# Kernel tuning notes

Hardware: AMD Instinct MI355X
Metric: run time of the kernel (lower is better)

Reference implementation:

```python
import jax, jax.numpy as jnp
import numpy as np
from jax import lax

B = 2
K = 3          # class_num (out_channels)
EPS = 1e-5


def group_norm(x, gamma, beta, groups):
    # x: [B, C, D, W, H]
    b, c, d, w, h = x.shape
    xg = x.reshape(b, groups, c // groups, d, w, h)
    mu = xg.mean(axis=(2, 3, 4, 5), keepdims=True)
    var = xg.var(axis=(2, 3, 4, 5), keepdims=True)
    xg = (xg - mu) * lax.rsqrt(var + EPS)
    x = xg.reshape(b, c, d, w, h)
    return x * gamma[None, :, None, None, None] + beta[None, :, None, None, None]


def setup_inputs() -> dict:
    key = jax.random.key(0)
    ks = jax.random.split(key, 16)
    s = 0.02
    inp = {
        "x_e": jax.random.normal(ks[0], (B, 128, 24, 24, 24), jnp.float32),
        "pred": jax.random.normal(ks[1], (B, 32, 96, 96, 96), jnp.float32),
        # GAP head params
        "gn_g": jnp.ones((128,), jnp.float32),
        "gn_b": jnp.zeros((128,), jnp.float32),
        "gap_w": jax.random.normal(ks[2], (256, 128, 3, 3, 3), jnp.float32) * s,
        "gap_b": jnp.zeros((256,), jnp.float32),
        # controller_first: Conv3d(512,512,1) == Linear
        "w_cf": jax.random.normal(ks[3], (512, 512), jnp.float32) * s,
        "b_cf": jnp.zeros((512,), jnp.float32),
        # controller: Conv3d(512,256,1)
        "w_c": jax.random.normal(ks[4], (256, 512), jnp.float32) * s,
        "b_c": jnp.zeros((256,), jnp.float32),
        # ProAttention(256, reduction=16): Linear(256,16) -> ReLU -> Linear(16,32)
        "w_a1": jax.random.normal(ks[5], (16, 256), jnp.float32) * s,
        "b_a1": jnp.zeros((16,), jnp.float32),
        "w_a2": jax.random.normal(ks[6], (32, 16), jnp.float32) * s,
        "b_a2": jnp.zeros((32,), jnp.float32),
        # organ embedding [K, 256]
        "emb": jax.random.normal(ks[7], (K, 256), jnp.float32),
        # three seg heads Conv3d(32,1,1): stacked [K, 32] weight, [K] bias
        "w_seg": jax.random.normal(ks[8], (K, 32), jnp.float32) * s,
        "b_seg": jnp.zeros((K,), jnp.float32),
    }
    return inp


def reference(x_e, pred, gn_g, gn_b, gap_w, gap_b, w_cf, b_cf, w_c, b_c,
              w_a1, b_a1, w_a2, b_a2, emb, w_seg, b_seg):
    # GAP(x_e.detach()): GroupNorm -> ReLU -> Conv3d(128->256, k3, s2, VALID) -> global avg pool
    xe = lax.stop_gradient(x_e)
    g = jax.nn.relu(group_norm(xe, gn_g, gn_b, groups=16))
    g = lax.conv_general_dilated(g, gap_w, window_strides=(2, 2, 2), padding="VALID",
                                 dimension_numbers=("NCDHW", "OIDHW", "NCDHW"))
    g = g + gap_b[None, :, None, None, None]
    x_feat = g.mean(axis=(2, 3, 4))                       # [B, 256]

    # per-sample: cat(repeat(x_feat), task_encoding) -> 1x1 conv heads, vectorized over B and K
    x_cond = jnp.concatenate(
        [jnp.broadcast_to(x_feat[:, None, :], (B, K, 256)),
         jnp.broadcast_to(emb[None, :, :], (B, K, 256))], axis=-1)          # [B, K, 512]
    p = jax.nn.relu(jnp.einsum("bkc,oc->bko", x_cond, w_cf) + b_cf)          # [B, K, 512]
    p_out = p                                                                 # returned as p_out in original
    c = jnp.einsum("bkc,oc->bko", p, w_c) + b_c                              # [B, K, 256]
    hid = jax.nn.relu(jnp.einsum("bkc,oc->bko", c, w_a1) + b_a1)             # [B, K, 16]
    gate = jax.nn.sigmoid(jnp.einsum("bkc,oc->bko", hid, w_a2) + b_a2)       # [B, K, 32]

    # out_k = Conv1x1_k(gate_k * pred) = sum_c gate[b,k,c]*w_seg[k,c]*pred[b,c] + b_seg[k]
    eff_w = gate * w_seg[None, :, :]                                          # [B, K, 32]
    logits = jnp.einsum("bkc,bcdwh->bkdwh", eff_w, pred) + b_seg[None, :, None, None, None]
    return logits  # [B, 3, 96, 96, 96]  (p_out available as intermediate `p`)
```

## Files before the change

kernel.cpp:

```cpp
#include <hip/hip_runtime.h>
#include <hip/hip_bf16.h>


#define NSPAT 13824
#define P4    221184

#define WS_STATSPART 0
#define WS_WINS      1024
#define WS_XF        28672
#define WS_P         29184
#define WS_C         32256
#define WS_EFFW      33792
#define WS_BAR       33984
#define WS_SINK      33992

__device__ __forceinline__ void spin_barrier(int* bar, int nb) {
  __syncthreads();
  if (threadIdx.x == 0) {
    __threadfence();
    int gen = atomicAdd(&bar[1], 0);
    int old = atomicAdd(&bar[0], 1);
    if (old == nb - 1) {
      atomicExch(&bar[0], 0);
      __threadfence();
      atomicAdd(&bar[1], 1);
    } else {
      while (atomicAdd(&bar[1], 0) == gen) __builtin_amdgcn_s_sleep(8);
    }
    __threadfence();
  }
  __syncthreads();
}

__global__ __launch_bounds__(256) void k1_stats_kernel(
    const float* __restrict__ x, const float* __restrict__ gap_w,
    const float* __restrict__ w_cf, const float* __restrict__ w_c,
    const float* __restrict__ w_a1, const float* __restrict__ emb,
    float* __restrict__ ws) {
  if (blockIdx.x == 0 && threadIdx.x == 0)
    atomicExch(&((int*)(ws + WS_BAR))[0], 0);
  if (blockIdx.x >= 512) {
    float s = 0.f;
    int tid = (blockIdx.x - 512) * 256 + threadIdx.x;
    const float4* g4 = (const float4*)gap_w;
    for (int i = tid; i < 221184; i += 16384) { float4 v = g4[i]; s += v.x + v.w; }
    const float4* a4 = (const float4*)w_cf;
    for (int i = tid; i < 65536;  i += 16384) { float4 v = a4[i]; s += v.x + v.w; }
    const float4* c4 = (const float4*)w_c;
    for (int i = tid; i < 32768;  i += 16384) { float4 v = c4[i]; s += v.x + v.w; }
    if (tid < 1024) { float4 v = ((const float4*)w_a1)[tid]; s += v.x; }
    if (tid < 192)  { float4 v = ((const float4*)emb)[tid];  s += v.x; }
    if (s == 1.2345e30f) ws[WS_SINK] = s;
    return;
  }
  int blk = blockIdx.x;
  const float4* p = (const float4*)(x + (size_t)blk * 6912);
  float s = 0.f, ss = 0.f;
  for (int i = threadIdx.x; i < 1728; i += 256) {
    float4 v = p[i];
    s  += v.x + v.y + v.z + v.w;
    ss += v.x*v.x + v.y*v.y + v.z*v.z + v.w*v.w;
  }
  #pragma unroll
  for (int off = 32; off; off >>= 1) {
    s  += __shfl_down(s, off);
    ss += __shfl_down(ss, off);
  }
  __shared__ float a[4], b2[4];
  int wid = threadIdx.x >> 6, lane = threadIdx.x & 63;
  if (lane == 0) { a[wid] = s; b2[wid] = ss; }
  __syncthreads();
  if (threadIdx.x == 0) {
    float2 r;
    r.x = a[0] + a[1] + a[2] + a[3];
    r.y = b2[0] + b2[1] + b2[2] + b2[3];
    ((float2*)(ws + WS_STATSPART))[blk] = r;
  }
}

__global__ __launch_bounds__(256) void k2_winsum_kernel(
    const float* __restrict__ x, const float* __restrict__ gn_g,
    const float* __restrict__ gn_b, float* __restrict__ ws) {
  int task = blockIdx.x;
  int zq = task & 3;
  int bc = task >> 2;
  int b = bc >> 7, c = bc & 127;
  int bg = b * 16 + (c >> 3);
  const float2* sp = (const float2*)(ws + WS_STATSPART) + bg * 16;
  float S = 0.f, SS = 0.f;
  #pragma unroll
  for (int j = 0; j < 16; j++) { float2 r = sp[j]; S += r.x; SS += r.y; }
  float mu   = S * (1.f / 110592.f);
  float var  = SS * (1.f / 110592.f) - mu * mu;
  float rstd = rsqrtf(var + 1e-5f);
  float ga = gn_g[c] * rstd;
  float be = gn_b[c] - mu * ga;

  __shared__ float smem[4140];
  int t = threadIdx.x;
  int nz     = (zq < 3) ? 3 : 2;
  int planes = 2 * nz + 1;
  int startf = zq * 3456;
  int nf4    = planes * 144;
  const float4* p = (const float4*)(x + (size_t)bc * NSPAT + startf);
  float4* l4 = (float4*)smem;
  for (int i = t; i < nf4; i += 256) {
    float4 v = p[i];
    float4 r;
    r.x = fmaxf(v.x * ga + be, 0.f);
    r.y = fmaxf(v.y * ga + be, 0.f);
    r.z = fmaxf(v.z * ga + be, 0.f);
    r.w = fmaxf(v.w * ga + be, 0.f);
    l4[i] = r;
  }
  __syncthreads();

  float acc[27];
  #pragma unroll
  for (int k = 0; k < 27; k++) acc[k] = 0.f;
  int npos = nz * 121;
  for (int pidx = t; pidx < npos; pidx += 256) {
    int zl = pidx / 121, rem = pidx % 121;
    int y = rem / 11, xx = rem % 11;
    int base = zl * 1152 + y * 48 + xx * 2;
    #pragma unroll
    for (int kz = 0; kz < 3; kz++)
      #pragma unroll
      for (int ky = 0; ky < 3; ky++)
        #pragma unroll
        for (int kx = 0; kx < 3; kx++)
          acc[kz * 9 + ky * 3 + kx] += smem[base + kz * 576 + ky * 24 + kx];
  }
  #pragma unroll
  for (int k = 0; k < 27; k++)
    for (int off = 32; off; off >>= 1)
      acc[k] += __shfl_down(acc[k], off);
  float* part = smem + 4032;
  __syncthreads();
  int wid = t >> 6, lane = t & 63;
  if (lane == 0)
    #pragma unroll
    for (int k = 0; k < 27; k++) part[wid * 27 + k] = acc[k];
  __syncthreads();
  if (t < 27) {
    float v = part[t] + part[27 + t] + part[54 + t] + part[81 + t];
    ws[WS_WINS + task * 27 + t] = v;
  }
}

__global__ __launch_bounds__(256) void k3_chain_kernel(
    const float* __restrict__ gap_w, const float* __restrict__ gap_b,
    const float* __restrict__ w_cf,  const float* __restrict__ b_cf,
    const float* __restrict__ w_c,   const float* __restrict__ b_c,
    const float* __restrict__ w_a1,  const float* __restrict__ b_a1,
    const float* __restrict__ w_a2,  const float* __restrict__ b_a2,
    const float* __restrict__ emb,   const float* __restrict__ w_seg,
    float* ws) {
  __shared__ float smem[3456];
  int* bar = (int*)(ws + WS_BAR);
  const int t   = threadIdx.x;
  const int blk = blockIdx.x;

  {
    int b = blk >> 6;
    int oc = blk & 63;
    const float* wp = ws + WS_WINS + b * 13824;
    for (int i = t; i < 3456; i += 256) {
      int c = i / 27, k = i - c * 27;
      const float* q = wp + c * 108 + k;
      smem[i] = q[0] + q[27] + q[54] + q[81];
    }
    __syncthreads();
    int olocal = t >> 6;
    int lane = t & 63;
    int o = oc * 4 + olocal;
    const float4* w4 = (const float4*)(gap_w + (size_t)o * 3456);
    const float4* s4 = (const float4*)smem;
    float acc = 0.f;
    for (int i = lane; i < 864; i += 64) {
      float4 wv = w4[i], sv = s4[i];
      acc += wv.x * sv.x + wv.y * sv.y + wv.z * sv.z + wv.w * sv.w;
    }
    #pragma unroll
    for (int off = 32; off; off >>= 1) acc += __shfl_down(acc, off);
    if (lane == 0) ws[WS_XF + b * 256 + o] = acc * (1.f / 1331.f) + gap_b[o];
  }
  spin_barrier(bar, 128);

  {
    for (int i = t; i < 1280; i += 256)
      smem[i] = (i < 512) ? ws[WS_XF + i] : emb[i - 512];
    __syncthreads();
    int r = t >> 6, lane = t & 63;
    int o = blk * 4 + r;
    const float4* w4  = (const float4*)(w_cf + (size_t)o * 512);
    const float4* xf4 = (const float4*)smem;
    const float4* em4 = (const float4*)(smem + 512);
    float4 wlo = w4[lane], whi = w4[lane + 64];
    float acc[6];
    #pragma unroll
    for (int bk = 0; bk < 6; bk++) {
      int b = (bk >= 3), k = bk - b * 3;
      float4 xv = xf4[b * 64 + lane];
      float4 ev = em4[k * 64 + lane];
      acc[bk] = wlo.x*xv.x + wlo.y*xv.y + wlo.z*xv.z + wlo.w*xv.w
              + whi.x*ev.x + whi.y*ev.y + whi.z*ev.z + whi.w*ev.w;
    }
    #pragma unroll
    for (int bk = 0; bk < 6; bk++)
      #pragma unroll
      for (int off = 32; off; off >>= 1)
        acc[bk] += __shfl_down(acc[bk], off);
    if (lane == 0) {
      float bb = b_cf[o];
      #pragma unroll
      for (int bk = 0; bk < 6; bk++)
        ws[WS_P + bk * 512 + o] = fmaxf(acc[bk] + bb, 0.f);
    }
  }
  spin_barrier(bar, 128);

  {
    for (int i = t; i < 3072; i += 256) smem[i] = ws[WS_P + i];
    __syncthreads();
    if (t < 128) {
      int r = t >> 6, lane = t & 63;
      int o = blk * 2 + r;
      const float4* w4 = (const float4*)(w_c + (size_t)o * 512);
      const float4* p4 = (const float4*)smem;
      float4 wlo = w4[lane], whi = w4[lane + 64];
      float acc[6];
      #pragma unroll
      for (int bk = 0; bk < 6; bk++) {
        float4 plo = p4[bk * 128 + lane];
        float4 phi = p4[bk * 128 + lane + 64];
        acc[bk] = wlo.x*plo.x + wlo.y*plo.y + wlo.z*plo.z + wlo.w*plo.w
                + whi.x*phi.x + whi.y*phi.y + whi.z*phi.z + whi.w*phi.w;
      }
      #pragma unroll
      for (int bk = 0; bk < 6; bk++)
        #pragma unroll
        for (int off = 32; off; off >>= 1)
          acc[bk] += __shfl_down(acc[bk], off);
      if (lane == 0) {
        float bb = b_c[o];
        #pragma unroll
        for (int bk = 0; bk < 6; bk++)
          ws[WS_C + bk * 256 + o] = acc[bk] + bb;
      }
    }
  }
  spin_barrier(bar, 128);

  if (blk == 0) {
    for (int i = t; i < 1536; i += 256) smem[i] = ws[WS_C + i];
    __syncthreads();
    __shared__ float hid[96];
    if (t < 96) {
      int bk = t >> 4, h = t & 15;
      const float4* w4 = (const float4*)(w_a1 + h * 256);
      const float4* c4 = (const float4*)(smem + bk * 256);
      float acc = b_a1[h];
      for (int j = 0; j < 64; j++) {
        float4 wv = w4[j], cv = c4[j];
        acc += wv.x*cv.x + wv.y*cv.y + wv.z*cv.z + wv.w*cv.w;
      }
      hid[bk * 16 + h] = fmaxf(acc, 0.f);
    }
    __syncthreads();
    if (t < 192) {
      int bk = t >> 5, o = t & 31;
      int k = bk - (bk >= 3) * 3;
      float acc = b_a2[o];
      #pragma unroll
      for (int j = 0; j < 16; j++) acc += w_a2[o * 16 + j] * hid[bk * 16 + j];
      float gate = 1.f / (1.f + __expf(-acc));
      ws[WS_EFFW + bk * 32 + o] = gate * w_seg[k * 32 + o];
    }
  }
}

__global__ __launch_bounds__(256) void k4_seg_kernel(
    const float* __restrict__ pred, const float* __restrict__ ws_in,
    const float* __restrict__ b_seg, float* __restrict__ out) {
  __shared__ float ew[192];
  if (threadIdx.x < 192) ew[threadIdx.x] = ws_in[WS_EFFW + threadIdx.x];
  __syncthreads();
  int gid = blockIdx.x * 256 + threadIdx.x;
  int b = gid / P4;
  int p = gid - b * P4;
  const float4* pr = (const float4*)pred + (size_t)b * 32 * P4 + p;
  const float* e = ew + b * 96;
  float4 a0 = {0, 0, 0, 0}, a1 = a0, a2 = a0;
  #pragma unroll 8
  for (int c = 0; c < 32; c++) {
    float4 v = pr[(size_t)c * P4];
    float w0 = e[c], w1 = e[32 + c], w2 = e[64 + c];
    a0.x += w0 * v.x; a0.y += w0 * v.y; a0.z += w0 * v.z; a0.w += w0 * v.w;
    a1.x += w1 * v.x; a1.y += w1 * v.y; a1.z += w1 * v.z; a1.w += w1 * v.w;
    a2.x += w2 * v.x; a2.y += w2 * v.y; a2.z += w2 * v.z; a2.w += w2 * v.w;
  }
  float s0 = b_seg[0], s1 = b_seg[1], s2 = b_seg[2];
  a0.x += s0; a0.y += s0; a0.z += s0; a0.w += s0;
  a1.x += s1; a1.y += s1; a1.z += s1; a1.w += s1;
  a2.x += s2; a2.y += s2; a2.z += s2; a2.w += s2;
  float4* o4 = (float4*)out + (size_t)b * 3 * P4 + p;
  o4[0]      = a0;
  o4[P4]     = a1;
  o4[2 * P4] = a2;
}

extern "C" void kernel_launch(void* const* d_in, const int* in_sizes, int n_in,
                              void* d_out, int out_size, void* d_ws, size_t ws_size,
                              hipStream_t stream) {
  const float* x_e   = (const float*)d_in[0];
  const float* pred  = (const float*)d_in[1];
  const float* gn_g  = (const float*)d_in[2];
  const float* gn_b  = (const float*)d_in[3];
  const float* gap_w = (const float*)d_in[4];
  const float* gap_b = (const float*)d_in[5];
  const float* w_cf  = (const float*)d_in[6];
  const float* b_cf  = (const float*)d_in[7];
  const float* w_c   = (const float*)d_in[8];
  const float* b_c   = (const float*)d_in[9];
  const float* w_a1  = (const float*)d_in[10];
  const float* b_a1  = (const float*)d_in[11];
  const float* w_a2  = (const float*)d_in[12];
  const float* b_a2  = (const float*)d_in[13];
  const float* emb   = (const float*)d_in[14];
  const float* w_seg = (const float*)d_in[15];
  const float* b_seg = (const float*)d_in[16];
  float* ws  = (float*)d_ws;
  float* out = (float*)d_out;

  k1_stats_kernel<<<576, 256, 0, stream>>>(x_e, gap_w, w_cf, w_c, w_a1, emb, ws);
  k2_winsum_kernel<<<1024, 256, 0, stream>>>(x_e, gn_g, gn_b, ws);
  k3_chain_kernel<<<128, 256, 0, stream>>>(gap_w, gap_b, w_cf, b_cf, w_c, b_c,
                                           w_a1, b_a1, w_a2, b_a2, emb, w_seg, ws);
  k4_seg_kernel<<<1728, 256, 0, stream>>>(pred, ws, b_seg, out);
}
```

Measured before the change: 114.8 us.

## Fuse stats, window-sum and MLP chain into one persistent kernel; nontemporal seg stores

Merges the GroupNorm statistics, the ReLU/window-sum pass and the controller chain into a single 256-block persistent kernel. Stages are separated by grid-wide spin barriers, and each block handles one whole (b,c) channel held in LDS, where before four z-slices were spread across blocks. This removes two kernel launches and the intermediate partial-sum round trips. The barrier is now reset with a hipMemsetAsync, and the weight-prefetch warmup is folded into the first stage. The seg kernel switches to nontemporal vector stores. The risks are fewer blocks doing the window-sum work, a larger LDS footprint that lowers occupancy, and deadlock if all 256 blocks are not co-resident.

```diff
diff --git a/kernel.cpp b/kernel.cpp
--- a/kernel.cpp
+++ b/kernel.cpp
@@ -2,17 +2,18 @@
 #include <hip/hip_bf16.h>
 
 
-#define NSPAT 13824
-#define P4    221184
+#define P4 221184
+
+typedef float v4f __attribute__((ext_vector_type(4)));
 
 #define WS_STATSPART 0
-#define WS_WINS      1024
-#define WS_XF        28672
-#define WS_P         29184
-#define WS_C         32256
-#define WS_EFFW      33792
-#define WS_BAR       33984
-#define WS_SINK      33992
+#define WS_WINS      512
+#define WS_XF        7424
+#define WS_P         7936
+#define WS_C         11008
+#define WS_EFFW      12544
+#define WS_BAR       12736
+#define WS_SINK      12740
 
 __device__ __forceinline__ void spin_barrier(int* bar, int nb) {
   __syncthreads();
@@ -32,123 +33,9 @@
   __syncthreads();
 }
 
-__global__ __launch_bounds__(256) void k1_stats_kernel(
-    const float* __restrict__ x, const float* __restrict__ gap_w,
-    const float* __restrict__ w_cf, const float* __restrict__ w_c,
-    const float* __restrict__ w_a1, const float* __restrict__ emb,
-    float* __restrict__ ws) {
-  if (blockIdx.x == 0 && threadIdx.x == 0)
-    atomicExch(&((int*)(ws + WS_BAR))[0], 0);
-  if (blockIdx.x >= 512) {
-    float s = 0.f;
-    int tid = (blockIdx.x - 512) * 256 + threadIdx.x;
-    const float4* g4 = (const float4*)gap_w;
-    for (int i = tid; i < 221184; i += 16384) { float4 v = g4[i]; s += v.x + v.w; }
-    const float4* a4 = (const float4*)w_cf;
-    for (int i = tid; i < 65536;  i += 16384) { float4 v = a4[i]; s += v.x + v.w; }
-    const float4* c4 = (const float4*)w_c;
-    for (int i = tid; i < 32768;  i += 16384) { float4 v = c4[i]; s += v.x + v.w; }
-    if (tid < 1024) { float4 v = ((const float4*)w_a1)[tid]; s += v.x; }
-    if (tid < 192)  { float4 v = ((const float4*)emb)[tid];  s += v.x; }
-    if (s == 1.2345e30f) ws[WS_SINK] = s;
-    return;
-  }
-  int blk = blockIdx.x;
-  const float4* p = (const float4*)(x + (size_t)blk * 6912);
-  float s = 0.f, ss = 0.f;
-  for (int i = threadIdx.x; i < 1728; i += 256) {
-    float4 v = p[i];
-    s  += v.x + v.y + v.z + v.w;
-    ss += v.x*v.x + v.y*v.y + v.z*v.z + v.w*v.w;
-  }
-  #pragma unroll
-  for (int off = 32; off; off >>= 1) {
-    s  += __shfl_down(s, off);
-    ss += __shfl_down(ss, off);
-  }
-  __shared__ float a[4], b2[4];
-  int wid = threadIdx.x >> 6, lane = threadIdx.x & 63;
-  if (lane == 0) { a[wid] = s; b2[wid] = ss; }
-  __syncthreads();
-  if (threadIdx.x == 0) {
-    float2 r;
-    r.x = a[0] + a[1] + a[2] + a[3];
-    r.y = b2[0] + b2[1] + b2[2] + b2[3];
-    ((float2*)(ws + WS_STATSPART))[blk] = r;
-  }
-}
-
-__global__ __launch_bounds__(256) void k2_winsum_kernel(
-    const float* __restrict__ x, const float* __restrict__ gn_g,
-    const float* __restrict__ gn_b, float* __restrict__ ws) {
-  int task = blockIdx.x;
-  int zq = task & 3;
-  int bc = task >> 2;
-  int b = bc >> 7, c = bc & 127;
-  int bg = b * 16 + (c >> 3);
-  const float2* sp = (const float2*)(ws + WS_STATSPART) + bg * 16;
-  float S = 0.f, SS = 0.f;
-  #pragma unroll
-  for (int j = 0; j < 16; j++) { float2 r = sp[j]; S += r.x; SS += r.y; }
-  float mu   = S * (1.f / 110592.f);
-  float var  = SS * (1.f / 110592.f) - mu * mu;
-  float rstd = rsqrtf(var + 1e-5f);
-  float ga = gn_g[c] * rstd;
-  float be = gn_b[c] - mu * ga;
-
-  __shared__ float smem[4140];
-  int t = threadIdx.x;
-  int nz     = (zq < 3) ? 3 : 2;
-  int planes = 2 * nz + 1;
-  int startf = zq * 3456;
-  int nf4    = planes * 144;
-  const float4* p = (const float4*)(x + (size_t)bc * NSPAT + startf);
-  float4* l4 = (float4*)smem;
-  for (int i = t; i < nf4; i += 256) {
-    float4 v = p[i];
-    float4 r;
-    r.x = fmaxf(v.x * ga + be, 0.f);
-    r.y = fmaxf(v.y * ga + be, 0.f);
-    r.z = fmaxf(v.z * ga + be, 0.f);
-    r.w = fmaxf(v.w * ga + be, 0.f);
-    l4[i] = r;
-  }
-  __syncthreads();
-
-  float acc[27];
-  #pragma unroll
-  for (int k = 0; k < 27; k++) acc[k] = 0.f;
-  int npos = nz * 121;
-  for (int pidx = t; pidx < npos; pidx += 256) {
-    int zl = pidx / 121, rem = pidx % 121;
-    int y = rem / 11, xx = rem % 11;
-    int base = zl * 1152 + y * 48 + xx * 2;
-    #pragma unroll
-    for (int kz = 0; kz < 3; kz++)
-      #pragma unroll
-      for (int ky = 0; ky < 3; ky++)
-        #pragma unroll
-        for (int kx = 0; kx < 3; kx++)
-          acc[kz * 9 + ky * 3 + kx] += smem[base + kz * 576 + ky * 24 + kx];
-  }
-  #pragma unroll
-  for (int k = 0; k < 27; k++)
-    for (int off = 32; off; off >>= 1)
-      acc[k] += __shfl_down(acc[k], off);
-  float* part = smem + 4032;
-  __syncthreads();
-  int wid = t >> 6, lane = t & 63;
-  if (lane == 0)
-    #pragma unroll
-    for (int k = 0; k < 27; k++) part[wid * 27 + k] = acc[k];
-  __syncthreads();
-  if (t < 27) {
-    float v = part[t] + part[27 + t] + part[54 + t] + part[81 + t];
-    ws[WS_WINS + task * 27 + t] = v;
-  }
-}
-
-__global__ __launch_bounds__(256) void k3_chain_kernel(
+__global__ __launch_bounds__(256) void chain_kernel(
+    const float* __restrict__ x_e,
+    const float* __restrict__ gn_g, const float* __restrict__ gn_b,
     const float* __restrict__ gap_w, const float* __restrict__ gap_b,
     const float* __restrict__ w_cf,  const float* __restrict__ b_cf,
     const float* __restrict__ w_c,   const float* __restrict__ b_c,
@@ -156,24 +43,106 @@
     const float* __restrict__ w_a2,  const float* __restrict__ b_a2,
     const float* __restrict__ emb,   const float* __restrict__ w_seg,
     float* ws) {
-  __shared__ float smem[3456];
+  __shared__ float smem[13932];
   int* bar = (int*)(ws + WS_BAR);
   const int t   = threadIdx.x;
   const int blk = blockIdx.x;
 
   {
-    int b = blk >> 6;
-    int oc = blk & 63;
-    const float* wp = ws + WS_WINS + b * 13824;
+    const float4* p = (const float4*)(x_e + (size_t)blk * 13824);
+    float s = 0.f, ss = 0.f;
     for (int i = t; i < 3456; i += 256) {
-      int c = i / 27, k = i - c * 27;
-      const float* q = wp + c * 108 + k;
-      smem[i] = q[0] + q[27] + q[54] + q[81];
-    }
-    __syncthreads();
-    int olocal = t >> 6;
-    int lane = t & 63;
-    int o = oc * 4 + olocal;
+      float4 v = p[i];
+      s  += v.x + v.y + v.z + v.w;
+      ss += v.x*v.x + v.y*v.y + v.z*v.z + v.w*v.w;
+    }
+    #pragma unroll
+    for (int off = 32; off; off >>= 1) {
+      s  += __shfl_down(s, off);
+      ss += __shfl_down(ss, off);
+    }
+    if ((t & 63) == 0) { smem[(t >> 6) * 2] = s; smem[(t >> 6) * 2 + 1] = ss; }
+    float sink = 0.f;
+    int tid = blk * 256 + t;
+    const float4* g4 = (const float4*)gap_w;
+    for (int i = tid; i < 221184; i += 65536) { float4 v = g4[i]; sink += v.x + v.w; }
+    if (tid < 65536) { float4 v = ((const float4*)w_cf)[tid]; sink += v.x + v.w; }
+    if (tid < 32768) { float4 v = ((const float4*)w_c)[tid];  sink += v.x + v.w; }
+    if (tid < 1024)  { float4 v = ((const float4*)w_a1)[tid]; sink += v.x; }
+    if (tid < 192)   { float4 v = ((const float4*)emb)[tid];  sink += v.x; }
+    __syncthreads();
+    if (t == 0) {
+      float2 r;
+      r.x = smem[0] + smem[2] + smem[4] + smem[6];
+      r.y = smem[1] + smem[3] + smem[5] + smem[7];
+      ((float2*)(ws + WS_STATSPART))[blk] = r;
+    }
+    if (sink == 1.2345e30f) ws[WS_SINK] = sink;
+  }
+  spin_barrier(bar, 256);
+
+  {
+    int b = blk >> 7, c = blk & 127;
+    int bg = b * 16 + (c >> 3);
+    const float2* sp = (const float2*)(ws + WS_STATSPART) + bg * 8;
+    float S = 0.f, SS = 0.f;
+    #pragma unroll
+    for (int j = 0; j < 8; j++) { float2 r = sp[j]; S += r.x; SS += r.y; }
+    float mu   = S * (1.f / 110592.f);
+    float var  = SS * (1.f / 110592.f) - mu * mu;
+    float rstd = rsqrtf(var + 1e-5f);
+    float ga = gn_g[c] * rstd;
+    float be = gn_b[c] - mu * ga;
+
+    const float4* p = (const float4*)(x_e + (size_t)blk * 13824);
+    float4* l4 = (float4*)smem;
+    for (int i = t; i < 3456; i += 256) {
+      float4 v = p[i];
+      float4 r;
+      r.x = fmaxf(v.x * ga + be, 0.f);
+      r.y = fmaxf(v.y * ga + be, 0.f);
+      r.z = fmaxf(v.z * ga + be, 0.f);
+      r.w = fmaxf(v.w * ga + be, 0.f);
+      l4[i] = r;
+    }
+    __syncthreads();
+
+    float acc[27];
+    #pragma unroll
+    for (int k = 0; k < 27; k++) acc[k] = 0.f;
+    for (int pidx = t; pidx < 1331; pidx += 256) {
+      int z = pidx / 121, rem = pidx % 121;
+      int y = rem / 11, xx = rem % 11;
+      int base = z * 1152 + y * 48 + xx * 2;
+      #pragma unroll
+      for (int kz = 0; kz < 3; kz++)
+        #pragma unroll
+        for (int ky = 0; ky < 3; ky++)
+          #pragma unroll
+          for (int kx = 0; kx < 3; kx++)
+            acc[kz * 9 + ky * 3 + kx] += smem[base + kz * 576 + ky * 24 + kx];
+    }
+    #pragma unroll
+    for (int k = 0; k < 27; k++)
+      for (int off = 32; off; off >>= 1)
+        acc[k] += __shfl_down(acc[k], off);
+    float* part = smem + 13824;
+    int wid = t >> 6, lane = t & 63;
+    if (lane == 0)
+      #pragma unroll
+      for (int k = 0; k < 27; k++) part[wid * 27 + k] = acc[k];
+    __syncthreads();
+    if (t < 27)
+      ws[WS_WINS + blk * 27 + t] = part[t] + part[27 + t] + part[54 + t] + part[81 + t];
+  }
+  spin_barrier(bar, 256);
+
+  if (blk < 128) {
+    int b = blk >> 6, oc = blk & 63;
+    const float* wp = ws + WS_WINS + b * 3456;
+    for (int i = t; i < 3456; i += 256) smem[i] = wp[i];
+    __syncthreads();
+    int o = oc * 4 + (t >> 6), lane = t & 63;
     const float4* w4 = (const float4*)(gap_w + (size_t)o * 3456);
     const float4* s4 = (const float4*)smem;
     float acc = 0.f;
@@ -185,14 +154,13 @@
     for (int off = 32; off; off >>= 1) acc += __shfl_down(acc, off);
     if (lane == 0) ws[WS_XF + b * 256 + o] = acc * (1.f / 1331.f) + gap_b[o];
   }
-  spin_barrier(bar, 128);
-
-  {
+  spin_barrier(bar, 256);
+
+  if (blk < 128) {
     for (int i = t; i < 1280; i += 256)
       smem[i] = (i < 512) ? ws[WS_XF + i] : emb[i - 512];
     __syncthreads();
-    int r = t >> 6, lane = t & 63;
-    int o = blk * 4 + r;
+    int o = blk * 4 + (t >> 6), lane = t & 63;
     const float4* w4  = (const float4*)(w_cf + (size_t)o * 512);
     const float4* xf4 = (const float4*)smem;
     const float4* em4 = (const float4*)(smem + 512);
@@ -218,14 +186,13 @@
         ws[WS_P + bk * 512 + o] = fmaxf(acc[bk] + bb, 0.f);
     }
   }
-  spin_barrier(bar, 128);
-
-  {
+  spin_barrier(bar, 256);
+
+  if (blk < 128) {
     for (int i = t; i < 3072; i += 256) smem[i] = ws[WS_P + i];
     __syncthreads();
     if (t < 128) {
-      int r = t >> 6, lane = t & 63;
-      int o = blk * 2 + r;
+      int o = blk * 2 + (t >> 6), lane = t & 63;
       const float4* w4 = (const float4*)(w_c + (size_t)o * 512);
       const float4* p4 = (const float4*)smem;
       float4 wlo = w4[lane], whi = w4[lane + 64];
@@ -250,12 +217,12 @@
       }
     }
   }
-  spin_barrier(bar, 128);
+  spin_barrier(bar, 256);
 
   if (blk == 0) {
     for (int i = t; i < 1536; i += 256) smem[i] = ws[WS_C + i];
     __syncthreads();
-    __shared__ float hid[96];
+    float* hid = smem + 1536;
     if (t < 96) {
       int bk = t >> 4, h = t & 15;
       const float4* w4 = (const float4*)(w_a1 + h * 256);
@@ -280,7 +247,7 @@
   }
 }
 
-__global__ __launch_bounds__(256) void k4_seg_kernel(
+__global__ __launch_bounds__(256) void seg_kernel(
     const float* __restrict__ pred, const float* __restrict__ ws_in,
     const float* __restrict__ b_seg, float* __restrict__ out) {
   __shared__ float ew[192];
@@ -291,7 +258,7 @@
   int p = gid - b * P4;
   const float4* pr = (const float4*)pred + (size_t)b * 32 * P4 + p;
   const float* e = ew + b * 96;
-  float4 a0 = {0, 0, 0, 0}, a1 = a0, a2 = a0;
+  v4f a0 = {0, 0, 0, 0}, a1 = a0, a2 = a0;
   #pragma unroll 8
   for (int c = 0; c < 32; c++) {
     float4 v = pr[(size_t)c * P4];
@@ -301,13 +268,13 @@
     a2.x += w2 * v.x; a2.y += w2 * v.y; a2.z += w2 * v.z; a2.w += w2 * v.w;
   }
   float s0 = b_seg[0], s1 = b_seg[1], s2 = b_seg[2];
-  a0.x += s0; a0.y += s0; a0.z += s0; a0.w += s0;
-  a1.x += s1; a1.y += s1; a1.z += s1; a1.w += s1;
-  a2.x += s2; a2.y += s2; a2.z += s2; a2.w += s2;
-  float4* o4 = (float4*)out + (size_t)b * 3 * P4 + p;
-  o4[0]      = a0;
-  o4[P4]     = a1;
-  o4[2 * P4] = a2;
+  a0 += s0;
+  a1 += s1;
+  a2 += s2;
+  v4f* o4 = (v4f*)out + (size_t)b * 3 * P4 + p;
+  __builtin_nontemporal_store(a0, o4);
+  __builtin_nontemporal_store(a1, o4 + P4);
+  __builtin_nontemporal_store(a2, o4 + 2 * P4);
 }
 
 extern "C" void kernel_launch(void* const* d_in, const int* in_sizes, int n_in,
@@ -333,9 +300,9 @@
   float* ws  = (float*)d_ws;
   float* out = (float*)d_out;
 
-  k1_stats_kernel<<<576, 256, 0, stream>>>(x_e, gap_w, w_cf, w_c, w_a1, emb, ws);
-  k2_winsum_kernel<<<1024, 256, 0, stream>>>(x_e, gn_g, gn_b, ws);
-  k3_chain_kernel<<<128, 256, 0, stream>>>(gap_w, gap_b, w_cf, b_cf, w_c, b_c,
-                                           w_a1, b_a1, w_a2, b_a2, emb, w_seg, ws);
-  k4_seg_kernel<<<1728, 256, 0, stream>>>(pred, ws, b_seg, out);
+  (void)hipMemsetAsync((char*)d_ws + WS_BAR * 4, 0, 8, stream);
+  chain_kernel<<<256, 256, 0, stream>>>(x_e, gn_g, gn_b, gap_w, gap_b,
+                                        w_cf, b_cf, w_c, b_c, w_a1, b_a1,
+                                        w_a2, b_a2, emb, w_seg, ws);
+  seg_kernel<<<1728, 256, 0, stream>>>(pred, ws, b_seg, out);
 }
```

New measurement: 172.6 us. 50.4% more time.
